# Optimization experiments

Hardware: AMD Instinct MI355X
Metric: run time of the kernel (lower is better)

## Reference

```python
import jax, jax.numpy as jnp
import numpy as np

BATCH = 2
TIME_N = 196
SPACE_F = 8
D_MODEL = 768
N_HEADS = 12
D_STATE = 16
DT_RANK = 48  # ceil(768/16)
D_CONV = 4
SEQ = 1 + TIME_N * SPACE_F


def _ln(x, w, b, eps=1e-5):
    m = x.mean(-1, keepdims=True)
    v = ((x - m) ** 2).mean(-1, keepdims=True)
    return (x - m) * jax.lax.rsqrt(v + eps) * w + b


def _silu(x):
    return x * jax.nn.sigmoid(x)


def _causal_conv(x, w, b):
    # x: (B, L, d); depthwise causal conv1d, kernel D_CONV, padding left
    L = x.shape[1]
    xp = jnp.pad(x, ((0, 0), (D_CONV - 1, 0), (0, 0)))
    return sum(xp[:, k:k + L, :] * w[:, k] for k in range(D_CONV)) + b


def _ssm(u, delta, A, Bm, C, Dp):
    # u, delta: (B,L,d); A: (d,N); Bm, C: (B,L,N)
    dA = jnp.exp(delta[..., None] * A)                    # (B,L,d,N)
    dBu = (delta * u)[..., None] * Bm[:, :, None, :]      # (B,L,d,N)
    B, L, d, N = dA.shape

    def step(h, inp):
        a, bu = inp
        h = a * h + bu
        return h, h

    _, hs = jax.lax.scan(step, jnp.zeros((B, d, N), dA.dtype),
                         (dA.transpose(1, 0, 2, 3), dBu.transpose(1, 0, 2, 3)))
    return jnp.einsum('lbdn,bln->bld', hs, C) + u * Dp


def _mamba_dir(xp, z, conv_w, conv_b, xproj_w, dt_w, dt_b, A_log, Dp, flip):
    if flip:
        xp = xp[:, ::-1]
        z = z[:, ::-1]
    xc = _silu(_causal_conv(xp, conv_w, conv_b))
    x_dbl = xc @ xproj_w.T
    dt = x_dbl[..., :DT_RANK]
    Bm = x_dbl[..., DT_RANK:DT_RANK + D_STATE]
    C = x_dbl[..., DT_RANK + D_STATE:]
    delta = jax.nn.softplus(dt @ dt_w.T + dt_b)
    y = _ssm(xc, delta, -jnp.exp(A_log), Bm, C, Dp) * _silu(z)
    if flip:
        y = y[:, ::-1]
    return y


def _mamba(x, in_w, cw, cb, xw, dw, db, Al, Dp, cwb, cbb, xwb, dwb, dbb, Alb, Dpb, out_w):
    # bimamba v2: forward scan + backward (flipped) scan, summed, then out_proj
    xz = x @ in_w.T
    xp, z = jnp.split(xz, 2, axis=-1)
    y = (_mamba_dir(xp, z, cw, cb, xw, dw, db, Al, Dp, False)
         + _mamba_dir(xp, z, cwb, cbb, xwb, dwb, dbb, Alb, Dpb, True))
    return y @ out_w.T


def _mha(x, in_w, in_b, out_w, out_b):
    # torch nn.MultiheadAttention default (batch_first=False):
    # x is (L, N, E); attention runs over dim 0 (L), dim 1 (N) is batch.
    L, N, E = x.shape
    hd = E // N_HEADS
    qkv = x @ in_w.T + in_b
    q, k, v = jnp.split(qkv, 3, axis=-1)
    q = q.reshape(L, N, N_HEADS, hd)
    k = k.reshape(L, N, N_HEADS, hd)
    v = v.reshape(L, N, N_HEADS, hd)
    scores = jnp.einsum('lnhk,mnhk->nhlm', q, k) / jnp.sqrt(jnp.asarray(hd, x.dtype))
    o = jnp.einsum('nhlm,mnhk->lnhk', jax.nn.softmax(scores, axis=-1), v)
    return o.reshape(L, N, E) @ out_w.T + out_b


def _forward(x, norm1_w, norm1_b, norm2_w, norm2_b, norm3_w, norm3_b,
             attn_in_w, attn_in_b, attn_out_w, attn_out_b,
             m_in_w, m_conv_w, m_conv_b, m_xproj_w, m_dt_w, m_dt_b, m_Alog, m_D,
             m_conv_wb, m_conv_bb, m_xproj_wb, m_dt_wb, m_dt_bb, m_Alog_b, m_D_b,
             m_out_w, fc1_w, fc1_b, fc2_w, fc2_b, time_n, space_f):
    b, _, d = x.shape
    init_cls = x[:, :1]
    res_x = x
    # 'b (n t) d -> (b n) t d'
    xt = x[:, 1:].reshape(b, time_n, space_f, d).reshape(b * time_n, space_f, d)
    time_out = _mamba(_ln(xt, norm3_w, norm3_b), m_in_w, m_conv_w, m_conv_b,
                      m_xproj_w, m_dt_w, m_dt_b, m_Alog, m_D,
                      m_conv_wb, m_conv_bb, m_xproj_wb, m_dt_wb, m_dt_bb,
                      m_Alog_b, m_D_b, m_out_w)
    time_res = (xt + time_out).reshape(b, time_n, space_f, d)
    # cls repeat: 'b t d -> (b t) 1 d'
    cls = jnp.repeat(init_cls, space_f, axis=1).reshape(b * space_f, 1, d)
    # 'b (n t) d -> (b t) n d'
    xs = time_res.transpose(0, 2, 1, 3).reshape(b * space_f, time_n, d)
    xs = jnp.concatenate([cls, xs], axis=1)  # (b*t, n+1, d)
    space_out = _mha(_ln(xs, norm1_w, norm1_b), attn_in_w, attn_in_b, attn_out_w, attn_out_b)
    cls_tok = space_out[:, 0].reshape(b, space_f, d).mean(1, keepdims=True)
    # '(b t) n d -> b (n t) d'
    sp = space_out[:, 1:].reshape(b, space_f, time_n, d).transpose(0, 2, 1, 3).reshape(b, time_n * space_f, d)
    x = res_x + jnp.concatenate([cls_tok, sp], axis=1)
    h = _ln(x, norm2_w, norm2_b)
    h = jax.nn.gelu(h @ fc1_w.T + fc1_b, approximate=False) @ fc2_w.T + fc2_b
    return x + h


def setup_inputs():
    ks = iter(jax.random.split(jax.random.key(0), 64))

    def nrm(shape, s=0.02):
        return jax.random.normal(next(ks), shape, dtype=jnp.float32) * s

    d = D_MODEL
    Alog = jnp.log(jnp.tile(jnp.arange(1, D_STATE + 1, dtype=jnp.float32), (d, 1)))
    return dict(
        x=jax.random.normal(next(ks), (BATCH, SEQ, d), dtype=jnp.float32),
        norm1_w=jnp.ones((d,), jnp.float32), norm1_b=jnp.zeros((d,), jnp.float32),
        norm2_w=jnp.ones((d,), jnp.float32), norm2_b=jnp.zeros((d,), jnp.float32),
        norm3_w=jnp.ones((d,), jnp.float32), norm3_b=jnp.zeros((d,), jnp.float32),
        attn_in_w=nrm((3 * d, d)), attn_in_b=nrm((3 * d,)),
        attn_out_w=nrm((d, d)), attn_out_b=nrm((d,)),
        m_in_w=nrm((2 * d, d)),
        m_conv_w=nrm((d, D_CONV), 0.2), m_conv_b=nrm((d,), 0.1),
        m_xproj_w=nrm((DT_RANK + 2 * D_STATE, d)),
        m_dt_w=nrm((d, DT_RANK), 0.1), m_dt_b=nrm((d,), 0.5),
        m_Alog=Alog, m_D=jnp.ones((d,), jnp.float32),
        m_conv_wb=nrm((d, D_CONV), 0.2), m_conv_bb=nrm((d,), 0.1),
        m_xproj_wb=nrm((DT_RANK + 2 * D_STATE, d)),
        m_dt_wb=nrm((d, DT_RANK), 0.1), m_dt_bb=nrm((d,), 0.5),
        m_Alog_b=Alog, m_D_b=jnp.ones((d,), jnp.float32),
        m_out_w=nrm((d, d)),
        fc1_w=nrm((4 * d, d)), fc1_b=nrm((4 * d,), 0.01),
        fc2_w=nrm((d, 4 * d)), fc2_b=nrm((d,), 0.01),
        time_n=TIME_N, space_f=SPACE_F,
    )


def reference(x, norm1_w, norm1_b, norm2_w, norm2_b, norm3_w, norm3_b,
              attn_in_w, attn_in_b, attn_out_w, attn_out_b,
              m_in_w, m_conv_w, m_conv_b, m_xproj_w, m_dt_w, m_dt_b, m_Alog, m_D,
              m_conv_wb, m_conv_bb, m_xproj_wb, m_dt_wb, m_dt_bb, m_Alog_b, m_D_b,
              m_out_w, fc1_w, fc1_b, fc2_w, fc2_b, time_n, space_f):
    return _forward(x, norm1_w, norm1_b, norm2_w, norm2_b, norm3_w, norm3_b,
                    attn_in_w, attn_in_b, attn_out_w, attn_out_b,
                    m_in_w, m_conv_w, m_conv_b, m_xproj_w, m_dt_w, m_dt_b, m_Alog, m_D,
                    m_conv_wb, m_conv_bb, m_xproj_wb, m_dt_wb, m_dt_bb, m_Alog_b, m_D_b,
                    m_out_w, fc1_w, fc1_b, fc2_w, fc2_b, time_n, space_f)
```

## Files before the change

### kernel.cpp

```cpp
#include <hip/hip_runtime.h>
#include <hip/hip_bf16.h>
#include <math.h>

#define DM 768
#define NBATCH 2
#define TIMEN 196
#define SPACEF 8
#define SEQL 1569
#define NSTATE 16
#define MT 3136
#define NSEQ 392
#define AT 3152
#define XTOK 3138

typedef __attribute__((ext_vector_type(8))) short s16x8;
typedef __attribute__((ext_vector_type(4))) float f32x4;
typedef __hip_bfloat16 bf16;

__device__ __forceinline__ float silu_fast(float x){ return __fdividef(x, 1.0f + __expf(-x)); }
__device__ __forceinline__ float geluf(float x){
  float y = 0.7978845608f * (x + 0.044715f*x*x*x);
  float ay = fabsf(y);
  float e = __expf(-2.0f*ay);
  float t = __fdividef(1.0f - e, 1.0f + e);
  t = copysignf(t, y);
  return 0.5f*x*(1.0f + t);
}
__device__ __forceinline__ float softplusf(float x){
  return (x > 20.0f) ? x : __logf(1.0f + __expf(x));
}
__device__ __forceinline__ int imin(int a, int b){ return a < b ? a : b; }

#define GLD_LDS16(g, l) __builtin_amdgcn_global_load_lds( \
    (const __attribute__((address_space(1))) void*)(g), \
    (__attribute__((address_space(3))) void*)(l), 16, 0, 0)

template<int N, int K, int Np, int Kp>
__device__ __forceinline__ void cvt_seg(const float* __restrict__ src, bf16* __restrict__ dst){
  const int total = Np * Kp;
  int base = blockIdx.x * 1024 + threadIdx.x;
  #pragma unroll
  for (int e = 0; e < 4; e++){
    int idx = base + e * 256;
    if (idx < total){
      int n = idx / Kp, k = idx % Kp;
      float v = (n < N && k < K) ? src[n * K + k] : 0.0f;
      dst[idx] = __float2bfloat16(v);
    }
  }
}

__global__ __launch_bounds__(256) void cvtw_kernel(
    const float* s0, const float* s1, const float* s2, const float* s3,
    const float* s4, const float* s5, const float* s6, const float* s7,
    const float* s8, const float* s9, bf16* w)
{
  switch (blockIdx.y) {
    case 0: cvt_seg<1536,768,1536,768>(s0, w + 0);        break;
    case 1: cvt_seg<  80,768, 128,768>(s1, w + 1179648);  break;
    case 2: cvt_seg<  80,768, 128,768>(s2, w + 1277952);  break;
    case 3: cvt_seg< 768, 48, 768, 64>(s3, w + 1376256);  break;
    case 4: cvt_seg< 768, 48, 768, 64>(s4, w + 1425408);  break;
    case 5: cvt_seg< 768,768, 768,768>(s5, w + 1474560);  break;
    case 6: cvt_seg<2304,768,2304,768>(s6, w + 2064384);  break;
    case 7: cvt_seg< 768,768, 768,768>(s7, w + 3833856);  break;
    case 8: cvt_seg<3072,768,3072,768>(s8, w + 4423680);  break;
    default:cvt_seg< 768,3072,768,3072>(s9, w + 6782976); break;
  }
}

__device__ __forceinline__ float block_sum256(float v, float* sm){
  #pragma unroll
  for (int o = 32; o > 0; o >>= 1) v += __shfl_down(v, o);
  __syncthreads();
  if ((threadIdx.x & 63) == 0) sm[threadIdx.x >> 6] = v;
  __syncthreads();
  return sm[0] + sm[1] + sm[2] + sm[3];
}

__global__ __launch_bounds__(256) void ln_kernel(
    const float* __restrict__ src0, const float* __restrict__ src1,
    const float* __restrict__ w, const float* __restrict__ b,
    bf16* __restrict__ out, int mode)
{
  __shared__ float sm[4];
  int tok = blockIdx.x;
  const float* src;
  if (mode == 0) {
    src = src0 + (size_t)tok * DM;
  } else if (mode == 1) {
    int bi = tok / (TIMEN*SPACEF), r = tok % (TIMEN*SPACEF);
    src = src0 + ((size_t)bi * SEQL + 1 + r) * DM;
  } else {
    int sidx = tok / 197, p = tok % 197;
    if (p == 0) src = src0 + (size_t)(sidx >> 3) * SEQL * DM;
    else { int bi = sidx >> 3, f = sidx & 7, t = p - 1;
           src = src1 + (size_t)((bi*TIMEN + t)*SPACEF + f) * DM; }
  }
  int tid = threadIdx.x;
  float xr[3];
  #pragma unroll
  for (int i = 0; i < 3; i++) xr[i] = src[tid + i*256];
  float mean = block_sum256(xr[0]+xr[1]+xr[2], sm) * (1.0f/768.0f);
  float v0 = xr[0]-mean, v1 = xr[1]-mean, v2 = xr[2]-mean;
  float var = block_sum256(v0*v0 + v1*v1 + v2*v2, sm) * (1.0f/768.0f);
  float rstd = rsqrtf(var + 1e-5f);
  bf16* o = out + (size_t)tok * DM;
  #pragma unroll
  for (int i = 0; i < 3; i++){ int c = tid + i*256;
    o[c] = __float2bfloat16((xr[i]-mean)*rstd*w[c] + b[c]); }
}

template<int BM, int BN>
__global__ __launch_bounds__(256) void mgemm(
    const bf16* __restrict__ A, int lda,
    const bf16* __restrict__ W0, const bf16* __restrict__ W1, int ldw,
    const float* __restrict__ bias0, const float* __restrict__ bias1,
    const float* __restrict__ resid,
    void* __restrict__ Cout, int M, int mhalf, int N, int ldc, int KP,
    int act, int resmode, int outbf16, int skw)
{
  constexpr int WM = BM/2, WN = BN/2, MI = WM/16, NJ = WN/16;
  __shared__ bf16 As[2][BM*64];
  __shared__ bf16 Bs[2][BN*64];
  int tid = threadIdx.x;
  int wave = tid >> 6, lane = tid & 63;

  int nwg = gridDim.x * gridDim.y;
  int bid = blockIdx.y * gridDim.x + blockIdx.x;
  int q = nwg >> 3, r = nwg & 7;
  int xcd = bid & 7, lidx = bid >> 3;
  int wg = (xcd < r ? xcd*(q+1) : r*(q+1) + (xcd-r)*q) + lidx;
  int m0 = (wg / gridDim.x) * BM, n0 = (wg % gridDim.x) * BN;

  int wr = wave >> 1, wc = wave & 1;

  int koff = blockIdx.z * KP;
  const bf16* Ak = A + koff;
  const bf16* Wt = ((m0 < mhalf) ? W0 : W1) + koff;
  const float* bias = (m0 < mhalf) ? bias0 : bias1;

  f32x4 acc[MI][NJ];
  #pragma unroll
  for (int i = 0; i < MI; i++)
    #pragma unroll
    for (int j = 0; j < NJ; j++) acc[i][j] = (f32x4){0.f,0.f,0.f,0.f};

  int sr8 = lane >> 3;
  int scs = (((lane & 7) ^ sr8) * 8);
  int lr16 = lane & 15, ks = (lane >> 4) * 8;
  int swz = (lr16 & 7) << 3;

  auto stage = [&](int buf, int k0){
    #pragma unroll
    for (int g = 0; g < BM/32; g++){
      int rr = wave*(BM/4) + g*8;
      const bf16* ga = Ak + (size_t)imin(m0 + rr + sr8, M-1)*lda + k0 + scs;
      GLD_LDS16(ga, &As[buf][rr*64]);
    }
    #pragma unroll
    for (int g = 0; g < BN/32; g++){
      int rr = wave*(BN/4) + g*8;
      const bf16* gb = Wt + (size_t)(n0 + rr + sr8)*ldw + k0 + scs;
      GLD_LDS16(gb, &Bs[buf][rr*64]);
    }
  };

  auto compute = [&](int buf){
    s16x8 afr[2][MI], bfr[2][NJ];
    #pragma unroll
    for (int kk = 0; kk < 2; kk++){
      #pragma unroll
      for (int i = 0; i < MI; i++)
        afr[kk][i] = *(const s16x8*)&As[buf][(wr*WM + i*16 + lr16)*64 + ((kk*32 + ks) ^ swz)];
      #pragma unroll
      for (int j = 0; j < NJ; j++)
        bfr[kk][j] = *(const s16x8*)&Bs[buf][(wc*WN + j*16 + lr16)*64 + ((kk*32 + ks) ^ swz)];
    }
    #pragma unroll
    for (int kk = 0; kk < 2; kk++)
      #pragma unroll
      for (int i = 0; i < MI; i++)
        #pragma unroll
        for (int j = 0; j < NJ; j++)
          acc[i][j] = __builtin_amdgcn_mfma_f32_16x16x32_bf16(afr[kk][i], bfr[kk][j], acc[i][j], 0, 0, 0);
  };

  stage(0, 0);
  __syncthreads();
  int cur = 0;
  for (int k0 = 64; k0 < KP; k0 += 64){
    stage(cur ^ 1, k0);
    compute(cur);
    __syncthreads();
    cur ^= 1;
  }
  compute(cur);

  #pragma unroll
  for (int i = 0; i < MI; i++){
    int rowb = m0 + wr*WM + i*16 + (lane >> 4)*4;
    #pragma unroll
    for (int j = 0; j < NJ; j++){
      int col = n0 + wc*WN + j*16 + lr16;
      if (col >= N) continue;
      float bv = bias ? bias[col] : 0.0f;
      #pragma unroll
      for (int r2 = 0; r2 < 4; r2++){
        int row = rowb + r2;
        if (row >= M) continue;
        float v = acc[i][j][r2];
        if (skw > 1){
          ((float*)Cout)[((size_t)(blockIdx.z*M) + row)*ldc + col] = v;
          continue;
        }
        v += bv;
        if (act == 1) v = geluf(v);
        else if (act == 2) v = softplusf(v);
        if (resmode == 1) v += resid[(size_t)row*ldc + col];
        else if (resmode == 2){
          int bi = row / (TIMEN*SPACEF), rr = row % (TIMEN*SPACEF);
          v += resid[((size_t)bi*SEQL + 1 + rr)*DM + col];
        }
        if (outbf16) ((bf16*)Cout)[(size_t)row*ldc + col] = __float2bfloat16(v);
        else         ((float*)Cout)[(size_t)row*ldc + col] = v;
      }
    }
  }
}

__global__ __launch_bounds__(256) void redk(
    const float* __restrict__ part, const float* __restrict__ bias,
    const float* __restrict__ resid, float* __restrict__ out,
    int M, int sk, int resmode)
{
  int i = blockIdx.x*256 + threadIdx.x;
  if (i*4 >= M*768) return;
  int row = i / 192;
  int c4 = (i - row*192) * 4;
  size_t base = (size_t)row*768 + c4;
  float4 v = *(const float4*)(part + base);
  for (int z = 1; z < sk; z++){
    float4 p = *(const float4*)(part + (size_t)z*M*768 + base);
    v.x += p.x; v.y += p.y; v.z += p.z; v.w += p.w;
  }
  if (bias){
    float4 b = *(const float4*)(bias + c4);
    v.x += b.x; v.y += b.y; v.z += b.z; v.w += b.w;
  }
  if (resmode == 1){
    float4 r = *(const float4*)(resid + base);
    v.x += r.x; v.y += r.y; v.z += r.z; v.w += r.w;
  } else if (resmode == 2){
    int bi = row / (TIMEN*SPACEF), rr = row % (TIMEN*SPACEF);
    float4 r = *(const float4*)(resid + ((size_t)bi*SEQL + 1 + rr)*DM + c4);
    v.x += r.x; v.y += r.y; v.z += r.z; v.w += r.w;
  }
  *(float4*)(out + base) = v;
}

__global__ __launch_bounds__(256) void conv_kernel(
    const float* __restrict__ xz,
    const float* __restrict__ wf, const float* __restrict__ bf,
    const float* __restrict__ wb, const float* __restrict__ bb,
    bf16* __restrict__ xcf, bf16* __restrict__ xcb)
{
  int g = blockIdx.x*256 + threadIdx.x;
  if (g >= NSEQ*DM) return;
  int s = g / DM, d = g % DM;
  float xr[8];
  #pragma unroll
  for (int j = 0; j < 8; j++) xr[j] = xz[(size_t)(s*8 + j)*1536 + d];
  float wfv[4], wbv[4];
  #pragma unroll
  for (int k = 0; k < 4; k++){ wfv[k] = wf[d*4+k]; wbv[k] = wb[d*4+k]; }
  float bfv = bf[d], bbv = bb[d];
  #pragma unroll
  for (int l = 0; l < 8; l++) {
    float af = bfv, ab = bbv;
    #pragma unroll
    for (int k = 0; k < 4; k++) {
      if (l + k >= 3) {
        af += wfv[k] * xr[l + k - 3];
        ab += wbv[k] * xr[10 - l - k];
      }
    }
    xcf[(size_t)(s*8 + l)*DM + d] = __float2bfloat16(silu_fast(af));
    xcb[(size_t)(s*8 + l)*DM + d] = __float2bfloat16(silu_fast(ab));
  }
}

__global__ __launch_bounds__(256) void ssm_kernel(
    const float* __restrict__ xz,
    const bf16* __restrict__ xcf, const bf16* __restrict__ xcb,
    const bf16* __restrict__ dblf, const bf16* __restrict__ dblb,
    const bf16* __restrict__ dlf, const bf16* __restrict__ dlb,
    const float* __restrict__ Alogf, const float* __restrict__ Df,
    const float* __restrict__ Alogb, const float* __restrict__ Db,
    bf16* __restrict__ y)
{
  int s = blockIdx.y;
  int d = blockIdx.x*256 + threadIdx.x;
  int tid = threadIdx.x;
  __shared__ float sBC[2][8][32];
  #pragma unroll
  for (int i = 0; i < 2; i++){
    int idx = tid + i*256;
    int dir = idx >> 8, r = idx & 255, l = r >> 5, j = r & 31;
    const bf16* p = dir ? dblb : dblf;
    sBC[dir][l][j] = __bfloat162float(p[(size_t)(s*8 + l)*80 + 48 + j]);
  }
  float Af[NSTATE], Ab[NSTATE];
  #pragma unroll
  for (int n = 0; n < NSTATE; n++) {
    Af[n] = -__expf(Alogf[d*NSTATE + n]);
    Ab[n] = -__expf(Alogb[d*NSTATE + n]);
  }
  float Dfv = Df[d], Dbv = Db[d];
  __syncthreads();

  float hf[NSTATE] = {}, hb[NSTATE] = {};
  float yf[8], yb[8];
  #pragma unroll
  for (int l = 0; l < 8; l++) {
    int t = s*8 + l;
    float delf = __bfloat162float(dlf[(size_t)t*DM + d]);
    float uf   = __bfloat162float(xcf[(size_t)t*DM + d]);
    float duf  = delf * uf;
    float accf = 0.0f;
    #pragma unroll
    for (int n = 0; n < NSTATE; n++) {
      hf[n] = __expf(delf*Af[n])*hf[n] + duf*sBC[0][l][n];
      accf += hf[n]*sBC[0][l][16+n];
    }
    yf[l] = accf + uf*Dfv;
    float delb = __bfloat162float(dlb[(size_t)t*DM + d]);
    float ub   = __bfloat162float(xcb[(size_t)t*DM + d]);
    float dub  = delb * ub;
    float accb = 0.0f;
    #pragma unroll
    for (int n = 0; n < NSTATE; n++) {
      hb[n] = __expf(delb*Ab[n])*hb[n] + dub*sBC[1][l][n];
      accb += hb[n]*sBC[1][l][16+n];
    }
    yb[7-l] = accb + ub*Dbv;
  }
  #pragma unroll
  for (int l = 0; l < 8; l++) {
    int t = s*8 + l;
    float zv = xz[(size_t)t*1536 + DM + d];
    y[(size_t)t*DM + d] = __float2bfloat16((yf[l] + yb[l]) * silu_fast(zv));
  }
}

__global__ __launch_bounds__(256) void attn_kernel(
    const bf16* __restrict__ qkv, bf16* __restrict__ ao)
{
  int n = blockIdx.x / 12, h = blockIdx.x % 12;
  __shared__ float qs[16][65], ks[16][65], vs[16][65], ps[16][17];
  int tid = threadIdx.x;
  for (int e = tid; e < 1024; e += 256) {
    int l = e >> 6, c = e & 63;
    size_t row = ((size_t)l*197 + n)*2304 + h*64 + c;
    qs[l][c] = __bfloat162float(qkv[row]);
    ks[l][c] = __bfloat162float(qkv[row + 768]);
    vs[l][c] = __bfloat162float(qkv[row + 1536]);
  }
  __syncthreads();
  int l = tid >> 4, m = tid & 15;
  float sc = 0.0f;
  #pragma unroll
  for (int c = 0; c < 64; c++) sc += qs[l][c]*ks[m][c];
  sc *= 0.125f;
  float mx = sc;
  #pragma unroll
  for (int o = 8; o > 0; o >>= 1) mx = fmaxf(mx, __shfl_xor(mx, o, 16));
  float p = __expf(sc - mx);
  float smv = p;
  #pragma unroll
  for (int o = 8; o > 0; o >>= 1) smv += __shfl_xor(smv, o, 16);
  ps[l][m] = __fdividef(p, smv);
  __syncthreads();
  for (int e = tid; e < 1024; e += 256) {
    int ll = e >> 6, c = e & 63;
    float acc = 0.0f;
    #pragma unroll
    for (int mm = 0; mm < 16; mm++) acc += ps[ll][mm]*vs[mm][c];
    ao[((size_t)ll*197 + n)*768 + h*64 + c] = __float2bfloat16(acc);
  }
}

__global__ __launch_bounds__(256) void scatter_kernel(
    const float* __restrict__ x, const float* __restrict__ so,
    float* __restrict__ xnew)
{
  int idx = blockIdx.x*256 + threadIdx.x;
  if (idx >= NBATCH*SEQL*DM) return;
  int bi = idx / (SEQL*DM);
  int rem = idx % (SEQL*DM);
  int row = rem / DM, d = rem % DM;
  float v;
  if (row == 0) {
    float acc = 0.0f;
    #pragma unroll
    for (int f = 0; f < SPACEF; f++)
      acc += so[((size_t)(bi*SPACEF + f)*197)*DM + d];
    v = x[idx] + acc * 0.125f;
  } else {
    int t = (row - 1) >> 3, f = (row - 1) & 7;
    v = x[idx] + so[((size_t)(bi*SPACEF + f)*197 + 1 + t)*DM + d];
  }
  xnew[idx] = v;
}

extern "C" void kernel_launch(void* const* d_in, const int* in_sizes, int n_in,
                              void* d_out, int out_size, void* d_ws, size_t ws_size,
                              hipStream_t stream) {
  const float* x        = (const float*)d_in[0];
  const float* norm1_w  = (const float*)d_in[1];
  const float* norm1_b  = (const float*)d_in[2];
  const float* norm2_w  = (const float*)d_in[3];
  const float* norm2_b  = (const float*)d_in[4];
  const float* norm3_w  = (const float*)d_in[5];
  const float* norm3_b  = (const float*)d_in[6];
  const float* attn_in_w  = (const float*)d_in[7];
  const float* attn_in_b  = (const float*)d_in[8];
  const float* attn_out_w = (const float*)d_in[9];
  const float* attn_out_b = (const float*)d_in[10];
  const float* m_in_w   = (const float*)d_in[11];
  const float* m_conv_w = (const float*)d_in[12];
  const float* m_conv_b = (const float*)d_in[13];
  const float* m_xproj_w= (const float*)d_in[14];
  const float* m_dt_w   = (const float*)d_in[15];
  const float* m_dt_b   = (const float*)d_in[16];
  const float* m_Alog   = (const float*)d_in[17];
  const float* m_D      = (const float*)d_in[18];
  const float* m_conv_wb= (const float*)d_in[19];
  const float* m_conv_bb= (const float*)d_in[20];
  const float* m_xproj_wb=(const float*)d_in[21];
  const float* m_dt_wb  = (const float*)d_in[22];
  const float* m_dt_bb  = (const float*)d_in[23];
  const float* m_Alog_b = (const float*)d_in[24];
  const float* m_D_b    = (const float*)d_in[25];
  const float* m_out_w  = (const float*)d_in[26];
  const float* fc1_w    = (const float*)d_in[27];
  const float* fc1_b    = (const float*)d_in[28];
  const float* fc2_w    = (const float*)d_in[29];
  const float* fc2_b    = (const float*)d_in[30];

  char* wsb = (char*)d_ws;
  bf16*  wpool  = (bf16*)(wsb + 0);
  bf16*  ln3    = (bf16*)(wsb + 18284544);
  float* xz     = (float*)(wsb + 23101440);
  bf16*  xcf    = (bf16*)(wsb + 42369024);
  bf16*  xcb    = (bf16*)(wsb + 47185920);
  bf16*  dblf   = (bf16*)(wsb + 52002816);
  bf16*  dblb   = (bf16*)(wsb + 52504576);
  bf16*  dlf    = (bf16*)(wsb + 53006336);
  bf16*  dlb    = (bf16*)(wsb + 57823232);
  bf16*  y      = ln3;
  float* tres   = (float*)(wsb + 62640128);
  float* part1  = (float*)(wsb + 23101440);
  bf16*  xsln   = (bf16*)(wsb + 23101440);
  float* so     = (float*)(wsb + 27942912);
  bf16*  qkv    = (bf16*)(wsb + 42369024);
  bf16*  ao     = (bf16*)(wsb + 18284544);
  float* part2  = (float*)(wsb + 42369024);
  float* xnew   = tres;
  bf16*  ln2o   = (bf16*)(wsb + 23101440);
  bf16*  h1     = (bf16*)(wsb + 42369024);
  float* part3  = (float*)(wsb + 18284544);

  bf16* w_in  = wpool + 0;
  bf16* w_xpf = wpool + 1179648;
  bf16* w_xpb = wpool + 1277952;
  bf16* w_dtf = wpool + 1376256;
  bf16* w_dtb = wpool + 1425408;
  bf16* w_out = wpool + 1474560;
  bf16* w_qkv = wpool + 2064384;
  bf16* w_ao  = wpool + 3833856;
  bf16* w_fc1 = wpool + 4423680;
  bf16* w_fc2 = wpool + 6782976;

  const int BIGM = 1 << 30;

  cvtw_kernel<<<dim3(2304, 10), 256, 0, stream>>>(
      m_in_w, m_xproj_w, m_xproj_wb, m_dt_w, m_dt_wb, m_out_w,
      attn_in_w, attn_out_w, fc1_w, fc2_w, wpool);

  ln_kernel<<<MT, 256, 0, stream>>>(x, nullptr, norm3_w, norm3_b, ln3, 1);
  mgemm<64,64><<<dim3(24, 49), 256, 0, stream>>>(ln3, DM, w_in, w_in, DM,
      nullptr, nullptr, nullptr, xz, MT, BIGM, 1536, 1536, DM, 0, 0, 0, 1);
  conv_kernel<<<(NSEQ*DM + 255)/256, 256, 0, stream>>>(
      xz, m_conv_w, m_conv_b, m_conv_wb, m_conv_bb, xcf, xcb);
  mgemm<64,64><<<dim3(2, 98), 256, 0, stream>>>(xcf, DM, w_xpf, w_xpb, DM,
      nullptr, nullptr, nullptr, dblf, 2*MT, MT, 80, 80, DM, 0, 0, 1, 1);
  mgemm<64,64><<<dim3(12, 98), 256, 0, stream>>>(dblf, 80, w_dtf, w_dtb, 64,
      m_dt_b, m_dt_bb, nullptr, dlf, 2*MT, MT, DM, DM, 64, 2, 0, 1, 1);
  ssm_kernel<<<dim3(3, NSEQ), 256, 0, stream>>>(
      xz, xcf, xcb, dblf, dblb, dlf, dlb, m_Alog, m_D, m_Alog_b, m_D_b, y);
  mgemm<64,64><<<dim3(12, 49, 2), 256, 0, stream>>>(y, DM, w_out, w_out, DM,
      nullptr, nullptr, nullptr, part1, MT, BIGM, DM, DM, 384, 0, 0, 0, 2);
  redk<<<2352, 256, 0, stream>>>(part1, nullptr, x, tres, MT, 2, 2);

  ln_kernel<<<AT, 256, 0, stream>>>(x, tres, norm1_w, norm1_b, xsln, 2);
  mgemm<64,64><<<dim3(36, 50), 256, 0, stream>>>(xsln, DM, w_qkv, w_qkv, DM,
      attn_in_b, attn_in_b, nullptr, qkv, AT, BIGM, 2304, 2304, DM, 0, 0, 1, 1);
  attn_kernel<<<197*12, 256, 0, stream>>>(qkv, ao);
  mgemm<64,64><<<dim3(12, 50, 2), 256, 0, stream>>>(ao, DM, w_ao, w_ao, DM,
      nullptr, nullptr, nullptr, part2, AT, BIGM, DM, DM, 384, 0, 0, 0, 2);
  redk<<<2364, 256, 0, stream>>>(part2, attn_out_b, nullptr, so, AT, 2, 0);
  scatter_kernel<<<(NBATCH*SEQL*DM + 255)/256, 256, 0, stream>>>(x, so, xnew);

  ln_kernel<<<XTOK, 256, 0, stream>>>(xnew, nullptr, norm2_w, norm2_b, ln2o, 0);
  mgemm<64,64><<<dim3(48, 50), 256, 0, stream>>>(ln2o, DM, w_fc1, w_fc1, DM,
      fc1_b, fc1_b, nullptr, h1, XTOK, BIGM, 3072, 3072, DM, 1, 0, 1, 1);
  mgemm<64,64><<<dim3(12, 50, 2), 256, 0, stream>>>(h1, 3072, w_fc2, w_fc2, 3072,
      nullptr, nullptr, nullptr, part3, XTOK, BIGM, DM, DM, 1536, 0, 0, 0, 2);
  redk<<<2354, 256, 0, stream>>>(part3, fc2_b, xnew, (float*)d_out, XTOK, 2, 1);
}
```

Baseline: 290.1 us.

## Fuse split-K reductions, residual scatter and layernorms; remap GEMM tiles per XCD

Two element-wise pass pairs are merged. The split-K reduction plus residual is folded into the following layernorm (redk_ln), and the attention-output reduction, bias, scatter and residual are folded into the norm2 layernorm (scatter_ln). This removes two launches and several full fp32 round trips of the activation tensors. The GEMM tile-to-workgroup mapping also gains a 2D block decomposition per XCD when the grid divides evenly, aiming for better L2 locality. The cost is extra register and address work in the fused kernels, and the redundant row-0 summation across 8 frames in scatter_ln.

```diff
diff --git a/kernel.cpp b/kernel.cpp
--- a/kernel.cpp
+++ b/kernel.cpp
@@ -79,24 +79,14 @@
 }
 
 __global__ __launch_bounds__(256) void ln_kernel(
-    const float* __restrict__ src0, const float* __restrict__ src1,
+    const float* __restrict__ src0,
     const float* __restrict__ w, const float* __restrict__ b,
-    bf16* __restrict__ out, int mode)
+    bf16* __restrict__ out)
 {
   __shared__ float sm[4];
   int tok = blockIdx.x;
-  const float* src;
-  if (mode == 0) {
-    src = src0 + (size_t)tok * DM;
-  } else if (mode == 1) {
-    int bi = tok / (TIMEN*SPACEF), r = tok % (TIMEN*SPACEF);
-    src = src0 + ((size_t)bi * SEQL + 1 + r) * DM;
-  } else {
-    int sidx = tok / 197, p = tok % 197;
-    if (p == 0) src = src0 + (size_t)(sidx >> 3) * SEQL * DM;
-    else { int bi = sidx >> 3, f = sidx & 7, t = p - 1;
-           src = src1 + (size_t)((bi*TIMEN + t)*SPACEF + f) * DM; }
-  }
+  int bi = tok / (TIMEN*SPACEF), r = tok % (TIMEN*SPACEF);
+  const float* src = src0 + ((size_t)bi * SEQL + 1 + r) * DM;
   int tid = threadIdx.x;
   float xr[3];
   #pragma unroll
@@ -106,6 +96,85 @@
   float var = block_sum256(v0*v0 + v1*v1 + v2*v2, sm) * (1.0f/768.0f);
   float rstd = rsqrtf(var + 1e-5f);
   bf16* o = out + (size_t)tok * DM;
+  #pragma unroll
+  for (int i = 0; i < 3; i++){ int c = tid + i*256;
+    o[c] = __float2bfloat16((xr[i]-mean)*rstd*w[c] + b[c]); }
+}
+
+__global__ __launch_bounds__(256) void redk_ln(
+    const float* __restrict__ part, const float* __restrict__ x,
+    const float* __restrict__ w, const float* __restrict__ b,
+    bf16* __restrict__ out)
+{
+  __shared__ float sm[4];
+  int tok = blockIdx.x;
+  int sidx = tok / 197, p = tok % 197;
+  int tid = threadIdx.x;
+  float xr[3];
+  if (p == 0) {
+    const float* src = x + (size_t)(sidx >> 3) * SEQL * DM;
+    #pragma unroll
+    for (int i = 0; i < 3; i++) xr[i] = src[tid + i*256];
+  } else {
+    int bi = sidx >> 3, f = sidx & 7, t = p - 1;
+    size_t mt = ((size_t)(bi*TIMEN + t))*SPACEF + f;
+    const float* p0 = part + mt*DM;
+    const float* p1 = part + ((size_t)MT + mt)*DM;
+    const float* xs = x + ((size_t)bi*SEQL + 1 + t*SPACEF + f)*DM;
+    #pragma unroll
+    for (int i = 0; i < 3; i++){ int c = tid + i*256;
+      xr[i] = p0[c] + p1[c] + xs[c]; }
+  }
+  float mean = block_sum256(xr[0]+xr[1]+xr[2], sm) * (1.0f/768.0f);
+  float v0 = xr[0]-mean, v1 = xr[1]-mean, v2 = xr[2]-mean;
+  float var = block_sum256(v0*v0 + v1*v1 + v2*v2, sm) * (1.0f/768.0f);
+  float rstd = rsqrtf(var + 1e-5f);
+  bf16* o = out + (size_t)tok * DM;
+  #pragma unroll
+  for (int i = 0; i < 3; i++){ int c = tid + i*256;
+    o[c] = __float2bfloat16((xr[i]-mean)*rstd*w[c] + b[c]); }
+}
+
+__global__ __launch_bounds__(256) void scatter_ln(
+    const float* __restrict__ part, const float* __restrict__ bias,
+    const float* __restrict__ x, float* __restrict__ xnew,
+    const float* __restrict__ w, const float* __restrict__ b,
+    bf16* __restrict__ out)
+{
+  __shared__ float sm[4];
+  int tok = blockIdx.x;
+  int bi = tok / SEQL, row = tok % SEQL;
+  int tid = threadIdx.x;
+  const float* p1 = part + (size_t)AT*DM;
+  const float* xs = x + (size_t)tok*DM;
+  float xr[3];
+  if (row == 0) {
+    #pragma unroll
+    for (int i = 0; i < 3; i++){ int c = tid + i*256;
+      float acc = 0.0f;
+      #pragma unroll
+      for (int f = 0; f < SPACEF; f++){
+        size_t r = ((size_t)(bi*SPACEF + f)*197)*DM + c;
+        acc += part[r] + p1[r];
+      }
+      xr[i] = xs[c] + acc * 0.125f + bias[c];
+    }
+  } else {
+    int t = (row - 1) >> 3, f = (row - 1) & 7;
+    size_t r = ((size_t)((bi*SPACEF + f)*197) + 1 + t)*DM;
+    #pragma unroll
+    for (int i = 0; i < 3; i++){ int c = tid + i*256;
+      xr[i] = xs[c] + part[r + c] + p1[r + c] + bias[c];
+    }
+  }
+  float* xo = xnew + (size_t)tok*DM;
+  #pragma unroll
+  for (int i = 0; i < 3; i++) xo[tid + i*256] = xr[i];
+  float mean = block_sum256(xr[0]+xr[1]+xr[2], sm) * (1.0f/768.0f);
+  float v0 = xr[0]-mean, v1 = xr[1]-mean, v2 = xr[2]-mean;
+  float var = block_sum256(v0*v0 + v1*v1 + v2*v2, sm) * (1.0f/768.0f);
+  float rstd = rsqrtf(var + 1e-5f);
+  bf16* o = out + (size_t)tok*DM;
   #pragma unroll
   for (int i = 0; i < 3; i++){ int c = tid + i*256;
     o[c] = __float2bfloat16((xr[i]-mean)*rstd*w[c] + b[c]); }
@@ -126,12 +195,22 @@
   int tid = threadIdx.x;
   int wave = tid >> 6, lane = tid & 63;
 
-  int nwg = gridDim.x * gridDim.y;
-  int bid = blockIdx.y * gridDim.x + blockIdx.x;
-  int q = nwg >> 3, r = nwg & 7;
-  int xcd = bid & 7, lidx = bid >> 3;
-  int wg = (xcd < r ? xcd*(q+1) : r*(q+1) + (xcd-r)*q) + lidx;
-  int m0 = (wg / gridDim.x) * BM, n0 = (wg % gridDim.x) * BN;
+  int gx = gridDim.x, gy = gridDim.y;
+  int nwg = gx * gy;
+  int bid = blockIdx.y * gx + blockIdx.x;
+  int m0, n0;
+  if ((gx & 3) == 0 && (gy & 1) == 0) {
+    int cw = gx >> 2, rh = gy >> 1;
+    int xcd = bid & 7, lidx = bid >> 3;
+    int rx = xcd & 3, ry = xcd >> 2;
+    m0 = ((ry * rh) + lidx / cw) * BM;
+    n0 = ((rx * cw) + lidx % cw) * BN;
+  } else {
+    int q = nwg >> 3, r = nwg & 7;
+    int xcd = bid & 7, lidx = bid >> 3;
+    int wg = (xcd < r ? xcd*(q+1) : r*(q+1) + (xcd-r)*q) + lidx;
+    m0 = (wg / gx) * BM; n0 = (wg % gx) * BN;
+  }
 
   int wr = wave >> 1, wc = wave & 1;
 
@@ -218,10 +297,6 @@
         if (act == 1) v = geluf(v);
         else if (act == 2) v = softplusf(v);
         if (resmode == 1) v += resid[(size_t)row*ldc + col];
-        else if (resmode == 2){
-          int bi = row / (TIMEN*SPACEF), rr = row % (TIMEN*SPACEF);
-          v += resid[((size_t)bi*SEQL + 1 + rr)*DM + col];
-        }
         if (outbf16) ((bf16*)Cout)[(size_t)row*ldc + col] = __float2bfloat16(v);
         else         ((float*)Cout)[(size_t)row*ldc + col] = v;
       }
@@ -232,7 +307,7 @@
 __global__ __launch_bounds__(256) void redk(
     const float* __restrict__ part, const float* __restrict__ bias,
     const float* __restrict__ resid, float* __restrict__ out,
-    int M, int sk, int resmode)
+    int M, int sk)
 {
   int i = blockIdx.x*256 + threadIdx.x;
   if (i*4 >= M*768) return;
@@ -244,18 +319,9 @@
     float4 p = *(const float4*)(part + (size_t)z*M*768 + base);
     v.x += p.x; v.y += p.y; v.z += p.z; v.w += p.w;
   }
-  if (bias){
-    float4 b = *(const float4*)(bias + c4);
-    v.x += b.x; v.y += b.y; v.z += b.z; v.w += b.w;
-  }
-  if (resmode == 1){
-    float4 r = *(const float4*)(resid + base);
-    v.x += r.x; v.y += r.y; v.z += r.z; v.w += r.w;
-  } else if (resmode == 2){
-    int bi = row / (TIMEN*SPACEF), rr = row % (TIMEN*SPACEF);
-    float4 r = *(const float4*)(resid + ((size_t)bi*SEQL + 1 + rr)*DM + c4);
-    v.x += r.x; v.y += r.y; v.z += r.z; v.w += r.w;
-  }
+  float4 bvec = *(const float4*)(bias + c4);
+  float4 r = *(const float4*)(resid + base);
+  v.x += bvec.x + r.x; v.y += bvec.y + r.y; v.z += bvec.z + r.z; v.w += bvec.w + r.w;
   *(float4*)(out + base) = v;
 }
 
@@ -388,29 +454,6 @@
     for (int mm = 0; mm < 16; mm++) acc += ps[ll][mm]*vs[mm][c];
     ao[((size_t)ll*197 + n)*768 + h*64 + c] = __float2bfloat16(acc);
   }
-}
-
-__global__ __launch_bounds__(256) void scatter_kernel(
-    const float* __restrict__ x, const float* __restrict__ so,
-    float* __restrict__ xnew)
-{
-  int idx = blockIdx.x*256 + threadIdx.x;
-  if (idx >= NBATCH*SEQL*DM) return;
-  int bi = idx / (SEQL*DM);
-  int rem = idx % (SEQL*DM);
-  int row = rem / DM, d = rem % DM;
-  float v;
-  if (row == 0) {
-    float acc = 0.0f;
-    #pragma unroll
-    for (int f = 0; f < SPACEF; f++)
-      acc += so[((size_t)(bi*SPACEF + f)*197)*DM + d];
-    v = x[idx] + acc * 0.125f;
-  } else {
-    int t = (row - 1) >> 3, f = (row - 1) & 7;
-    v = x[idx] + so[((size_t)(bi*SPACEF + f)*197 + 1 + t)*DM + d];
-  }
-  xnew[idx] = v;
 }
 
 extern "C" void kernel_launch(void* const* d_in, const int* in_sizes, int n_in,
@@ -459,14 +502,12 @@
   bf16*  dlf    = (bf16*)(wsb + 53006336);
   bf16*  dlb    = (bf16*)(wsb + 57823232);
   bf16*  y      = ln3;
-  float* tres   = (float*)(wsb + 62640128);
   float* part1  = (float*)(wsb + 23101440);
-  bf16*  xsln   = (bf16*)(wsb + 23101440);
-  float* so     = (float*)(wsb + 27942912);
+  bf16*  xsln   = (bf16*)(wsb + 62640128);
   bf16*  qkv    = (bf16*)(wsb + 42369024);
   bf16*  ao     = (bf16*)(wsb + 18284544);
   float* part2  = (float*)(wsb + 42369024);
-  float* xnew   = tres;
+  float* xnew   = (float*)(wsb + 62640128);
   bf16*  ln2o   = (bf16*)(wsb + 23101440);
   bf16*  h1     = (bf16*)(wsb + 42369024);
   float* part3  = (float*)(wsb + 18284544);
@@ -488,7 +529,7 @@
       m_in_w, m_xproj_w, m_xproj_wb, m_dt_w, m_dt_wb, m_out_w,
       attn_in_w, attn_out_w, fc1_w, fc2_w, wpool);
 
-  ln_kernel<<<MT, 256, 0, stream>>>(x, nullptr, norm3_w, norm3_b, ln3, 1);
+  ln_kernel<<<MT, 256, 0, stream>>>(x, norm3_w, norm3_b, ln3);
   mgemm<64,64><<<dim3(24, 49), 256, 0, stream>>>(ln3, DM, w_in, w_in, DM,
       nullptr, nullptr, nullptr, xz, MT, BIGM, 1536, 1536, DM, 0, 0, 0, 1);
   conv_kernel<<<(NSEQ*DM + 255)/256, 256, 0, stream>>>(
@@ -501,21 +542,19 @@
       xz, xcf, xcb, dblf, dblb, dlf, dlb, m_Alog, m_D, m_Alog_b, m_D_b, y);
   mgemm<64,64><<<dim3(12, 49, 2), 256, 0, stream>>>(y, DM, w_out, w_out, DM,
       nullptr, nullptr, nullptr, part1, MT, BIGM, DM, DM, 384, 0, 0, 0, 2);
-  redk<<<2352, 256, 0, stream>>>(part1, nullptr, x, tres, MT, 2, 2);
-
-  ln_kernel<<<AT, 256, 0, stream>>>(x, tres, norm1_w, norm1_b, xsln, 2);
+
+  redk_ln<<<AT, 256, 0, stream>>>(part1, x, norm1_w, norm1_b, xsln);
   mgemm<64,64><<<dim3(36, 50), 256, 0, stream>>>(xsln, DM, w_qkv, w_qkv, DM,
       attn_in_b, attn_in_b, nullptr, qkv, AT, BIGM, 2304, 2304, DM, 0, 0, 1, 1);
   attn_kernel<<<197*12, 256, 0, stream>>>(qkv, ao);
   mgemm<64,64><<<dim3(12, 50, 2), 256, 0, stream>>>(ao, DM, w_ao, w_ao, DM,
       nullptr, nullptr, nullptr, part2, AT, BIGM, DM, DM, 384, 0, 0, 0, 2);
-  redk<<<2364, 256, 0, stream>>>(part2, attn_out_b, nullptr, so, AT, 2, 0);
-  scatter_kernel<<<(NBATCH*SEQL*DM + 255)/256, 256, 0, stream>>>(x, so, xnew);
-
-  ln_kernel<<<XTOK, 256, 0, stream>>>(xnew, nullptr, norm2_w, norm2_b, ln2o, 0);
+
+  scatter_ln<<<XTOK, 256, 0, stream>>>(part2, attn_out_b, x, xnew,
+      norm2_w, norm2_b, ln2o);
   mgemm<64,64><<<dim3(48, 50), 256, 0, stream>>>(ln2o, DM, w_fc1, w_fc1, DM,
       fc1_b, fc1_b, nullptr, h1, XTOK, BIGM, 3072, 3072, DM, 1, 0, 1, 1);
   mgemm<64,64><<<dim3(12, 50, 2), 256, 0, stream>>>(h1, 3072, w_fc2, w_fc2, 3072,
       nullptr, nullptr, nullptr, part3, XTOK, BIGM, DM, DM, 1536, 0, 0, 0, 2);
-  redk<<<2354, 256, 0, stream>>>(part3, fc2_b, xnew, (float*)d_out, XTOK, 2, 1);
-}
+  redk<<<2354, 256, 0, stream>>>(part3, fc2_b, xnew, (float*)d_out, XTOK, 2);
+}
```

Result: faster. 269.9 us (-7.0%).
